# Kernel optimization log

Measured on AMD Instinct MI355X. Metric: run time of the kernel, lower is better.

## Reference

```python
import jax, jax.numpy as jnp
import numpy as np

HIDDEN = 1024
GMM = 16


def setup_inputs() -> dict:
    key = jax.random.key(0)
    ks = jax.random.split(key, 9)
    B, T, D, S = 16, 1024, HIDDEN, 512
    sc_ih = 1.0 / np.sqrt(2 * D)
    sc_hh = 1.0 / np.sqrt(D)
    return {
        "input_h_c": jax.random.normal(ks[0], (B, T, D), jnp.float32),
        "memory": jax.random.normal(ks[1], (B, S, D), jnp.float32),
        "input_lengths": jax.random.randint(ks[2], (B,), 1, S + 1),
        "W_ih": jax.random.uniform(ks[3], (4 * D, 2 * D), jnp.float32, -sc_ih, sc_ih),
        "W_hh": jax.random.uniform(ks[4], (4 * D, D), jnp.float32, -sc_hh, sc_hh),
        "b_ih": jax.random.uniform(ks[5], (4 * D,), jnp.float32, -sc_hh, sc_hh),
        "b_hh": jax.random.uniform(ks[6], (4 * D,), jnp.float32, -sc_hh, sc_hh),
        "Wg_w": jax.random.uniform(ks[7], (3 * GMM, D), jnp.float32, -sc_hh, sc_hh),
        "Wg_b": jax.random.uniform(ks[8], (3 * GMM,), jnp.float32, -sc_hh, sc_hh),
    }


def reference(input_h_c, memory, input_lengths, W_ih, W_hh, b_ih, b_hh, Wg_w, Wg_b):
    B, T, D = input_h_c.shape
    S = memory.shape[1]
    M = Wg_b.shape[0] // 3
    b = b_ih + b_hh
    u = jnp.arange(S, dtype=input_h_c.dtype)  # positions u

    def step(carry, x_t):
        h, c, ctx = carry
        x = jnp.concatenate([x_t, ctx], axis=-1)  # [B, 2D]
        gates = x @ W_ih.T + h @ W_hh.T + b  # [B, 4D], torch gate order i,f,g,o
        i_g, f_g, g_g, o_g = jnp.split(gates, 4, axis=-1)
        c = jax.nn.sigmoid(f_g) * c + jax.nn.sigmoid(i_g) * jnp.tanh(g_g)
        h = jax.nn.sigmoid(o_g) * jnp.tanh(c)
        phi = h @ Wg_w.T + Wg_b  # [B, 3M]
        ksi = jnp.exp(phi[:, :M])
        beta = jnp.exp(phi[:, M:2 * M])
        alpha = jax.nn.softmax(phi[:, 2 * M:], axis=-1)
        # 1/(1+exp((ksi-u)/beta)) == sigmoid((u-ksi)/beta)
        z = (u[None, None, :] - ksi[:, :, None]) / beta[:, :, None]  # [B,M,S]
        half = 0.5 / beta[:, :, None]
        F_R = jax.nn.sigmoid(z + half)  # CDF at u+0.5
        F_L = jax.nn.sigmoid(z - half)  # CDF at u-0.5
        w = jnp.einsum('bm,bms->bs', alpha, F_R - F_L)  # [B,S]
        term = 1.0 - jnp.einsum('bm,bms->bs', alpha, F_R)  # [B,S]
        ctx = jnp.einsum('bs,bsd->bd', w, memory)  # [B,D]
        return (h, c, ctx), (w, term)

    h0 = jnp.zeros((B, D), input_h_c.dtype)
    c0 = jnp.zeros((B, D), input_h_c.dtype)
    ctx0 = jnp.zeros((B, D), input_h_c.dtype)
    (h, c, ctx), (ws, terms) = jax.lax.scan(
        step, (h0, c0, ctx0), jnp.swapaxes(input_h_c, 0, 1))
    alignment = jnp.swapaxes(ws, 0, 1)  # [B,T,S]
    term_last = terms[-1]  # [B,S]
    termination = jnp.take_along_axis(term_last, (input_lengths - 1)[:, None], axis=1)  # [B,1]
    context = ctx[:, None, :]  # [B,1,D], last-step context (as returned by torch forward)
    return (context, alignment, termination)
```

## Files before the change

### kernel.cpp

```cpp
#include <hip/hip_runtime.h>
#include <hip/hip_fp16.h>

#define BB 16
#define TT 1024
#define DD 1024
#define SS 512
#define KK2 2048

#define NBLK 128
#define NTHR 512

#define OUT_ALIGN 16384
#define OUT_TERM  8404992

typedef __attribute__((ext_vector_type(8))) short short8;
typedef __attribute__((ext_vector_type(4))) float floatx4;
typedef __attribute__((ext_vector_type(2))) _Float16 half2v;

struct KParams {
  const float* x;
  const float* mem;
  const int*   lens;
  const float* W_ih;
  const float* W_hh;
  const float* b_ih;
  const float* b_hh;
  const float* Wg_w;
  const float* Wg_b;
  float* out;
  unsigned* bar;
  unsigned short* xc0;
  unsigned short* xc1;
};

__device__ __forceinline__ float sigf(float v) {
  return __builtin_amdgcn_rcpf(1.0f + __expf(-v));
}
__device__ __forceinline__ float tanhfast(float v) {
  float a = fabsf(v);
  float e = __expf(-2.0f * a);
  float r = (1.0f - e) * __builtin_amdgcn_rcpf(1.0f + e);
  return v < 0.0f ? -r : r;
}

__device__ __forceinline__ unsigned short f2bf(float f) {
  unsigned u = __float_as_uint(f);
  return (unsigned short)((u + 0x7FFFu + ((u >> 16) & 1u)) >> 16);
}
__device__ __forceinline__ unsigned pack2bf(float a, float b) {
  return (unsigned)f2bf(a) | ((unsigned)f2bf(b) << 16);
}
__device__ __forceinline__ unsigned cvtpk(float a, float b) {
  unsigned r;
  asm volatile("v_cvt_pk_bf16_f32 %0, %1, %2" : "=v"(r) : "v"(a), "v"(b));
  return r;
}

__device__ __forceinline__ void cstore_u32(unsigned* p2, unsigned v) {
  __hip_atomic_store(p2, v, __ATOMIC_RELAXED, __HIP_MEMORY_SCOPE_AGENT);
}
__device__ __forceinline__ unsigned cload_u32(const unsigned* p2) {
  return __hip_atomic_load(p2, __ATOMIC_RELAXED, __HIP_MEMORY_SCOPE_AGENT);
}
__device__ __forceinline__ unsigned long long cload_u64(const unsigned long long* p2) {
  return __hip_atomic_load(p2, __ATOMIC_RELAXED, __HIP_MEMORY_SCOPE_AGENT);
}

__device__ __forceinline__ void lds_barrier() {
  asm volatile("s_waitcnt lgkmcnt(0)\n\ts_barrier" ::: "memory");
}

__device__ __forceinline__ void grid_barrier(unsigned* bar, unsigned ep, int blk) {
  __syncthreads();
  if (threadIdx.x == 0) cstore_u32(&bar[64 + blk * 32], ep);
  if (threadIdx.x < NBLK) {
    while (cload_u32(&bar[64 + (int)threadIdx.x * 32]) < ep) __builtin_amdgcn_s_sleep(1);
  }
  __syncthreads();
}

union UF { unsigned w[4]; unsigned long long u[2]; short8 s; };

#define MFMA16 __builtin_amdgcn_mfma_f32_16x16x32_bf16

__device__ __forceinline__ void xh_mfma(const UF* xf, const UF* hf, const short8* bfr,
                                        floatx4& a00, floatx4& a01,
                                        floatx4& a10, floatx4& a11) {
  floatx4 z = {0.f, 0.f, 0.f, 0.f};
  a00 = z; a01 = z; a10 = z; a11 = z;
  a00 = MFMA16(xf[0].s, bfr[0],  a00, 0, 0, 0); a01 = MFMA16(xf[1].s, bfr[1],  a01, 0, 0, 0);
  a10 = MFMA16(xf[0].s, bfr[12], a10, 0, 0, 0); a11 = MFMA16(xf[1].s, bfr[13], a11, 0, 0, 0);
  a00 = MFMA16(xf[2].s, bfr[2],  a00, 0, 0, 0); a01 = MFMA16(xf[3].s, bfr[3],  a01, 0, 0, 0);
  a10 = MFMA16(xf[2].s, bfr[14], a10, 0, 0, 0); a11 = MFMA16(xf[3].s, bfr[15], a11, 0, 0, 0);
  a00 = MFMA16(hf[0].s, bfr[8],  a00, 0, 0, 0); a01 = MFMA16(hf[1].s, bfr[9],  a01, 0, 0, 0);
  a10 = MFMA16(hf[0].s, bfr[20], a10, 0, 0, 0); a11 = MFMA16(hf[1].s, bfr[21], a11, 0, 0, 0);
  a00 = MFMA16(hf[2].s, bfr[10], a00, 0, 0, 0); a01 = MFMA16(hf[3].s, bfr[11], a01, 0, 0, 0);
  a10 = MFMA16(hf[2].s, bfr[22], a10, 0, 0, 0); a11 = MFMA16(hf[3].s, bfr[23], a11, 0, 0, 0);
}

__device__ __forceinline__ float sel4(const floatx4& v, int r) {
  return (r == 0) ? v[0] : (r == 1) ? v[1] : (r == 2) ? v[2] : v[3];
}

__global__ __launch_bounds__(NTHR, 2) void tts_kernel(KParams p) {
  extern __shared__ char smem[];
  half2v* memsh2 = (half2v*)smem;

  __shared__ float redC[64 * 65 + 4];
  __shared__ float phiP[384];
  __shared__ float alsh[16], ksish[16], invbsh[16];
  __shared__ float Rsh[513];
  __shared__ half2v wsh2[256];
  __shared__ float ctxp[4][128];
  __shared__ float bsh48[48];

  const int t    = threadIdx.x;
  const int blk  = blockIdx.x;
  const int lane = t & 63;
  const int w    = t >> 6;
  const int bbt  = blk & 15;
  const int dc   = blk >> 4;

  short8 bfr[24];
  {
    const int n = lane & 15;
    const int q = lane >> 4;
#pragma unroll
    for (int nt = 0; nt < 2; ++nt) {
      const int r = (n & 3) * 1024 + blk * 8 + nt * 4 + (n >> 2);
#pragma unroll
      for (int ki = 0; ki < 12; ++ki) {
        short8 v;
        const int k0 = (ki >> 2) * 1024 + w * 128 + (ki & 3) * 32 + q * 8;
#pragma unroll
        for (int j = 0; j < 8; ++j) {
          int k = k0 + j;
          float wv = (k < 2048) ? p.W_ih[(size_t)r * 2048 + k]
                                : p.W_hh[(size_t)r * 1024 + (k - 2048)];
          v[j] = (short)f2bf(wv);
        }
        bfr[nt * 12 + ki] = v;
      }
    }
  }
  short8 wgB[12];
  {
    const int n = lane & 15;
    const int q = lane >> 4;
#pragma unroll
    for (int tau = 0; tau < 3; ++tau)
#pragma unroll
      for (int c = 0; c < 4; ++c) {
        short8 v;
        const float* wg = p.Wg_w + (size_t)(tau * 16 + n) * 1024 + w * 128 + c * 32 + q * 8;
#pragma unroll
        for (int j = 0; j < 8; ++j) v[j] = (short)f2bf(wg[j]);
        wgB[tau * 4 + c] = v;
      }
  }
  float biasreg[4] = {0.f, 0.f, 0.f, 0.f};
  if (t < 128) {
    int dl = t & 7;
#pragma unroll
    for (int g = 0; g < 4; ++g) {
      int r = g * 1024 + blk * 8 + dl;
      biasreg[g] = p.b_ih[r] + p.b_hh[r];
    }
  }
  if (t < 48) bsh48[t] = p.Wg_b[t];
  {
    int dl = t & 127, sp = t >> 7;
    for (int pr = sp; pr < 256; pr += 4) {
      const float* mp = p.mem + (size_t)bbt * SS * DD + (size_t)(2 * pr) * DD + dc * 128 + dl;
      half2v v;
      v.x = (_Float16)mp[0];
      v.y = (_Float16)mp[DD];
      memsh2[pr * 128 + dl] = v;
    }
  }

  float c_val = 0.0f;
  unsigned ep = 0;
  unsigned short* xc_cur = p.xc0;
  unsigned short* xc_nxt = p.xc1;
  const int ab2 = ((lane & 15) * KK2 + w * 128 + ((lane >> 4) * 8)) >> 2;
  const float* xrow = p.x + (size_t)(lane & 15) * TT * DD + w * 128 + ((lane >> 4) * 8);

  floatx4 acc00, acc01, acc10, acc11;
  {
    UF xf[4], hf[4];
#pragma unroll
    for (int sub = 0; sub < 4; ++sub) {
      floatx4 lo = *(const floatx4*)(xrow + sub * 32);
      floatx4 hi = *(const floatx4*)(xrow + sub * 32 + 4);
      xf[sub].w[0] = cvtpk(lo[0], lo[1]); xf[sub].w[1] = cvtpk(lo[2], lo[3]);
      xf[sub].w[2] = cvtpk(hi[0], hi[1]); xf[sub].w[3] = cvtpk(hi[2], hi[3]);
    }
    const unsigned long long* hb = (const unsigned long long*)p.xc0 + ab2 + 256;
#pragma unroll
    for (int sub = 0; sub < 4; ++sub) {
      hf[sub].u[0] = cload_u64(hb + sub * 8);
      hf[sub].u[1] = cload_u64(hb + sub * 8 + 1);
    }
    xh_mfma(xf, hf, bfr, acc00, acc01, acc10, acc11);
  }

  for (int tstep = 0; tstep < TT; ++tstep) {
    {
      const unsigned long long* cb = (const unsigned long long*)xc_cur + ab2;
      UF fc[4];
#pragma unroll
      for (int sub = 0; sub < 4; ++sub) {
        fc[sub].u[0] = cload_u64(cb + sub * 8);
        fc[sub].u[1] = cload_u64(cb + sub * 8 + 1);
      }
      floatx4 c00 = acc00, c01 = acc01, c10 = acc10, c11 = acc11;
      c00 = MFMA16(fc[0].s, bfr[4],  c00, 0, 0, 0); c01 = MFMA16(fc[1].s, bfr[5],  c01, 0, 0, 0);
      c10 = MFMA16(fc[0].s, bfr[16], c10, 0, 0, 0); c11 = MFMA16(fc[1].s, bfr[17], c11, 0, 0, 0);
      c00 = MFMA16(fc[2].s, bfr[6],  c00, 0, 0, 0); c01 = MFMA16(fc[3].s, bfr[7],  c01, 0, 0, 0);
      c10 = MFMA16(fc[2].s, bfr[18], c10, 0, 0, 0); c11 = MFMA16(fc[3].s, bfr[19], c11, 0, 0, 0);
      c00 += c01; c10 += c11;
#pragma unroll
      for (int reg = 0; reg < 4; ++reg) {
        redC[(w * 8 + reg) * 65 + lane]     = c00[reg];
        redC[(w * 8 + 4 + reg) * 65 + lane] = c10[reg];
      }
    }
    lds_barrier();
    if (t < 128) {
      int b = t >> 3, dl = t & 7, nt = dl >> 2, dl4 = dl & 3;
      int row = nt * 4 + (b & 3);
      float gate[4];
#pragma unroll
      for (int g = 0; g < 4; ++g) {
        int ls = ((b >> 2) << 4) | (dl4 * 4 + g);
        float s = biasreg[g];
#pragma unroll
        for (int w2 = 0; w2 < 8; ++w2) s += redC[(w2 * 8 + row) * 65 + ls];
        gate[g] = s;
      }
      c_val = sigf(gate[1]) * c_val + sigf(gate[0]) * tanhfast(gate[2]);
      float hv = sigf(gate[3]) * tanhfast(c_val);
      float hn = __shfl_down(hv, 1, 64);
      if ((t & 1) == 0)
        cstore_u32((unsigned*)(xc_nxt + b * KK2 + 1024 + blk * 8 + dl), pack2bf(hv, hn));
    }
    grid_barrier(p.bar, ++ep, blk);

    UF hf[4];
    {
      const unsigned long long* hb = (const unsigned long long*)xc_nxt + ab2 + 256;
#pragma unroll
      for (int sub = 0; sub < 4; ++sub) {
        hf[sub].u[0] = cload_u64(hb + sub * 8);
        hf[sub].u[1] = cload_u64(hb + sub * 8 + 1);
      }
    }
    UF xf[4];
    if (tstep + 1 < TT) {
      const float* xp = xrow + (size_t)(tstep + 1) * DD;
#pragma unroll
      for (int sub = 0; sub < 4; ++sub) {
        floatx4 lo = *(const floatx4*)(xp + sub * 32);
        floatx4 hi = *(const floatx4*)(xp + sub * 32 + 4);
        xf[sub].w[0] = cvtpk(lo[0], lo[1]); xf[sub].w[1] = cvtpk(lo[2], lo[3]);
        xf[sub].w[2] = cvtpk(hi[0], hi[1]); xf[sub].w[3] = cvtpk(hi[2], hi[3]);
      }
    }
    {
      floatx4 z = {0.f, 0.f, 0.f, 0.f};
      floatx4 ph0 = z, ph1 = z, ph2 = z;
      ph0 = MFMA16(hf[0].s, wgB[0], ph0, 0, 0, 0);
      ph1 = MFMA16(hf[0].s, wgB[4], ph1, 0, 0, 0);
      ph2 = MFMA16(hf[0].s, wgB[8], ph2, 0, 0, 0);
      ph0 = MFMA16(hf[1].s, wgB[1], ph0, 0, 0, 0);
      ph1 = MFMA16(hf[1].s, wgB[5], ph1, 0, 0, 0);
      ph2 = MFMA16(hf[1].s, wgB[9], ph2, 0, 0, 0);
      ph0 = MFMA16(hf[2].s, wgB[2], ph0, 0, 0, 0);
      ph1 = MFMA16(hf[2].s, wgB[6], ph1, 0, 0, 0);
      ph2 = MFMA16(hf[2].s, wgB[10], ph2, 0, 0, 0);
      ph0 = MFMA16(hf[3].s, wgB[3], ph0, 0, 0, 0);
      ph1 = MFMA16(hf[3].s, wgB[7], ph1, 0, 0, 0);
      ph2 = MFMA16(hf[3].s, wgB[11], ph2, 0, 0, 0);
      if ((lane >> 4) == (bbt >> 2)) {
        int m = lane & 15, r = bbt & 3;
        phiP[w * 48 + m]      = sel4(ph0, r);
        phiP[w * 48 + 16 + m] = sel4(ph1, r);
        phiP[w * 48 + 32 + m] = sel4(ph2, r);
      }
    }
    lds_barrier();
    if (t < 64) {
      float s = 0.f;
      if (t < 48) {
        s = bsh48[t];
#pragma unroll
        for (int i = 0; i < 8; ++i) s += phiP[i * 48 + t];
      }
      float mx = s;
#pragma unroll
      for (int o = 1; o < 16; o <<= 1) mx = fmaxf(mx, __shfl_xor(mx, o, 64));
      float e = __expf(s - mx);
      float sm = e;
#pragma unroll
      for (int o = 1; o < 16; o <<= 1) sm += __shfl_xor(sm, o, 64);
      float alpha_v = e * __builtin_amdgcn_rcpf(sm);
      float ksi_v   = __expf(s);
      float invb_v  = __expf(-s);
      if (t >= 32) { if (t < 48) alsh[t - 32] = alpha_v; }
      else if (t < 16) ksish[t] = ksi_v;
      else invbsh[t - 16] = invb_v;
      int m = t & 15;
      float am = __shfl(alpha_v, 32 + m, 64);
      float km = __shfl(ksi_v, m, 64);
      float bm = __shfl(invb_v, 16 + m, 64);
      float term = am * sigf((-0.5f - km) * bm);
#pragma unroll
      for (int o = 1; o < 16; o <<= 1) term += __shfl_xor(term, o, 64);
      if (t == 48) Rsh[0] = term;
    }
    lds_barrier();
    {
      float su = (float)t;
      float rv0 = 0.f, rv1 = 0.f;
#pragma unroll
      for (int m = 0; m < 16; m += 2) {
        rv0 += alsh[m]     * sigf((su + 0.5f - ksish[m])     * invbsh[m]);
        rv1 += alsh[m + 1] * sigf((su + 0.5f - ksish[m + 1]) * invbsh[m + 1]);
      }
      float rv = rv0 + rv1;
      float rvp = __shfl_up(rv, 1, 64);
      float rvn = __shfl_down(rv, 1, 64);
      Rsh[t + 1] = rv;
      if ((t & 1) == 0) {
        half2v v2;
        v2.x = (_Float16)(rv - rvp);
        v2.y = (_Float16)(rvn - rv);
        wsh2[t >> 1] = v2;
      }
      if (dc == 0 && (t & 63) != 0)
        p.out[OUT_ALIGN + ((size_t)bbt * TT + tstep) * SS + t] = rv - rvp;
    }
    lds_barrier();
    {
      if (dc == 0 && t < 8)
        p.out[OUT_ALIGN + ((size_t)bbt * TT + tstep) * SS + 64 * t] =
            Rsh[64 * t + 1] - Rsh[64 * t];
      if (tstep == TT - 1 && dc == 0 && t == 0)
        p.out[OUT_TERM + bbt] = 1.0f - Rsh[p.lens[bbt]];
      int dl = t & 127, sp = t >> 7;
      const int pb = sp * 64;
      half2v wa = wsh2[pb];       wa.x = (_Float16)(Rsh[2 * pb + 1] - Rsh[2 * pb]);
      half2v wb = wsh2[pb + 32];  wb.x = (_Float16)(Rsh[2 * pb + 65] - Rsh[2 * pb + 64]);
      float s0 = __builtin_amdgcn_fdot2(memsh2[pb * 128 + dl], wa, 0.f, false);
      float s1 = __builtin_amdgcn_fdot2(memsh2[(pb + 32) * 128 + dl], wb, 0.f, false);
#pragma unroll 8
      for (int q = 1; q < 32; ++q) {
        s0 = __builtin_amdgcn_fdot2(memsh2[(pb + q) * 128 + dl],      wsh2[pb + q],      s0, false);
        s1 = __builtin_amdgcn_fdot2(memsh2[(pb + 32 + q) * 128 + dl], wsh2[pb + 32 + q], s1, false);
      }
      ctxp[sp][dl] = s0 + s1;
    }
    lds_barrier();
    if (t < 128) {
      float cv = ctxp[0][t] + ctxp[1][t] + ctxp[2][t] + ctxp[3][t];
      if (tstep == TT - 1) p.out[bbt * DD + dc * 128 + t] = cv;
      float cvn = __shfl_down(cv, 1, 64);
      if ((t & 1) == 0)
        cstore_u32((unsigned*)(xc_nxt + bbt * KK2 + dc * 128 + t), pack2bf(cv, cvn));
    }
    __builtin_amdgcn_sched_barrier(0);
    if (tstep + 1 < TT) {
      xh_mfma(xf, hf, bfr, acc00, acc01, acc10, acc11);
    }
    grid_barrier(p.bar, ++ep, blk);

    unsigned short* tmp = xc_cur; xc_cur = xc_nxt; xc_nxt = tmp;
  }
}

extern "C" void kernel_launch(void* const* d_in, const int* in_sizes, int n_in,
                              void* d_out, int out_size, void* d_ws, size_t ws_size,
                              hipStream_t stream) {
  (void)in_sizes; (void)n_in; (void)out_size; (void)ws_size;
  KParams p;
  p.x    = (const float*)d_in[0];
  p.mem  = (const float*)d_in[1];
  p.lens = (const int*)d_in[2];
  p.W_ih = (const float*)d_in[3];
  p.W_hh = (const float*)d_in[4];
  p.b_ih = (const float*)d_in[5];
  p.b_hh = (const float*)d_in[6];
  p.Wg_w = (const float*)d_in[7];
  p.Wg_b = (const float*)d_in[8];
  p.out  = (float*)d_out;
  p.bar  = (unsigned*)d_ws;
  p.xc0  = (unsigned short*)((char*)d_ws + 36864);
  p.xc1  = (unsigned short*)((char*)d_ws + 36864 + 65536);

  hipMemsetAsync(d_ws, 0, 36864 + 65536, stream);

  const unsigned dynLds = 131072;
  hipFuncSetAttribute((const void*)tts_kernel, hipFuncAttributeMaxDynamicSharedMemorySize,
                      (int)dynLds);

  void* args[] = { &p };
  hipLaunchCooperativeKernel((const void*)tts_kernel, dim3(NBLK), dim3(NTHR), args, dynLds,
                             stream);
}
```

Baseline: 13.33 ms.

## Split grid barrier into arrive/wait with master-block release and overlap work

Replaces the all-to-all polling grid barrier with a split arrive/wait scheme. Block 0 polls every block's flag and publishes a single release flag, and the other blocks poll only that flag. The x-load/convert and next-step MFMA work are placed between arrive and wait to hide barrier latency. The gate/LSTM, phi and context-reduction epilogues are compacted into wave 0 so only one wave has to drain its stores before arriving. The cost is an extra hop through block 0 and a serialized single-wave epilogue, and correctness depends on the vmcnt wait being placed right.

```diff
diff --git a/kernel.cpp b/kernel.cpp
--- a/kernel.cpp
+++ b/kernel.cpp
@@ -70,13 +70,29 @@
   asm volatile("s_waitcnt lgkmcnt(0)\n\ts_barrier" ::: "memory");
 }
 
-__device__ __forceinline__ void grid_barrier(unsigned* bar, unsigned ep, int blk) {
-  __syncthreads();
-  if (threadIdx.x == 0) cstore_u32(&bar[64 + blk * 32], ep);
-  if (threadIdx.x < NBLK) {
-    while (cload_u32(&bar[64 + (int)threadIdx.x * 32]) < ep) __builtin_amdgcn_s_sleep(1);
-  }
-  __syncthreads();
+__device__ __forceinline__ void bar_arrive(unsigned* bar, unsigned ep, int blk,
+                                           int w, int lane) {
+  if (w == 0) {
+    asm volatile("s_waitcnt vmcnt(0)" ::: "memory");
+    if (lane == 0) cstore_u32(&bar[64 + blk * 32], ep);
+  }
+}
+__device__ __forceinline__ void bar_wait(unsigned* bar, unsigned ep, int blk,
+                                         int w, int lane) {
+  if (w == 0) {
+    if (blk == 0) {
+      for (;;) {
+        unsigned v0 = cload_u32(&bar[64 + lane * 32]);
+        unsigned v1 = cload_u32(&bar[64 + (lane + 64) * 32]);
+        if (v0 >= ep && v1 >= ep) break;
+        __builtin_amdgcn_s_sleep(1);
+      }
+      if (lane == 0) cstore_u32(&bar[0], ep);
+    } else if (lane == 0) {
+      while (cload_u32(&bar[0]) < ep) __builtin_amdgcn_s_sleep(1);
+    }
+  }
+  lds_barrier();
 }
 
 union UF { unsigned w[4]; unsigned long long u[2]; short8 s; };
@@ -158,14 +174,16 @@
         wgB[tau * 4 + c] = v;
       }
   }
-  float biasreg[4] = {0.f, 0.f, 0.f, 0.f};
-  if (t < 128) {
-    int dl = t & 7;
-#pragma unroll
-    for (int g = 0; g < 4; ++g) {
-      int r = g * 1024 + blk * 8 + dl;
-      biasreg[g] = p.b_ih[r] + p.b_hh[r];
-    }
+  float biasreg[2][4] = {{0.f, 0.f, 0.f, 0.f}, {0.f, 0.f, 0.f, 0.f}};
+  if (w == 0) {
+    int b8 = 2 * (lane & 3);
+#pragma unroll
+    for (int u = 0; u < 2; ++u)
+#pragma unroll
+      for (int g = 0; g < 4; ++g) {
+        int r = g * 1024 + blk * 8 + b8 + u;
+        biasreg[u][g] = p.b_ih[r] + p.b_hh[r];
+      }
   }
   if (t < 48) bsh48[t] = p.Wg_b[t];
   {
@@ -179,7 +197,7 @@
     }
   }
 
-  float c_val = 0.0f;
+  float cval[2] = {0.f, 0.f};
   unsigned ep = 0;
   unsigned short* xc_cur = p.xc0;
   unsigned short* xc_nxt = p.xc1;
@@ -188,21 +206,21 @@
 
   floatx4 acc00, acc01, acc10, acc11;
   {
-    UF xf[4], hf[4];
+    UF xf0[4], hf0[4];
 #pragma unroll
     for (int sub = 0; sub < 4; ++sub) {
       floatx4 lo = *(const floatx4*)(xrow + sub * 32);
       floatx4 hi = *(const floatx4*)(xrow + sub * 32 + 4);
-      xf[sub].w[0] = cvtpk(lo[0], lo[1]); xf[sub].w[1] = cvtpk(lo[2], lo[3]);
-      xf[sub].w[2] = cvtpk(hi[0], hi[1]); xf[sub].w[3] = cvtpk(hi[2], hi[3]);
+      xf0[sub].w[0] = cvtpk(lo[0], lo[1]); xf0[sub].w[1] = cvtpk(lo[2], lo[3]);
+      xf0[sub].w[2] = cvtpk(hi[0], hi[1]); xf0[sub].w[3] = cvtpk(hi[2], hi[3]);
     }
     const unsigned long long* hb = (const unsigned long long*)p.xc0 + ab2 + 256;
 #pragma unroll
     for (int sub = 0; sub < 4; ++sub) {
-      hf[sub].u[0] = cload_u64(hb + sub * 8);
-      hf[sub].u[1] = cload_u64(hb + sub * 8 + 1);
-    }
-    xh_mfma(xf, hf, bfr, acc00, acc01, acc10, acc11);
+      hf0[sub].u[0] = cload_u64(hb + sub * 8);
+      hf0[sub].u[1] = cload_u64(hb + sub * 8 + 1);
+    }
+    xh_mfma(xf0, hf0, bfr, acc00, acc01, acc10, acc11);
   }
 
   for (int tstep = 0; tstep < TT; ++tstep) {
@@ -227,35 +245,29 @@
       }
     }
     lds_barrier();
-    if (t < 128) {
-      int b = t >> 3, dl = t & 7, nt = dl >> 2, dl4 = dl & 3;
-      int row = nt * 4 + (b & 3);
-      float gate[4];
-#pragma unroll
-      for (int g = 0; g < 4; ++g) {
-        int ls = ((b >> 2) << 4) | (dl4 * 4 + g);
-        float s = biasreg[g];
-#pragma unroll
-        for (int w2 = 0; w2 < 8; ++w2) s += redC[(w2 * 8 + row) * 65 + ls];
-        gate[g] = s;
-      }
-      c_val = sigf(gate[1]) * c_val + sigf(gate[0]) * tanhfast(gate[2]);
-      float hv = sigf(gate[3]) * tanhfast(c_val);
-      float hn = __shfl_down(hv, 1, 64);
-      if ((t & 1) == 0)
-        cstore_u32((unsigned*)(xc_nxt + b * KK2 + 1024 + blk * 8 + dl), pack2bf(hv, hn));
-    }
-    grid_barrier(p.bar, ++ep, blk);
-
-    UF hf[4];
-    {
-      const unsigned long long* hb = (const unsigned long long*)xc_nxt + ab2 + 256;
-#pragma unroll
-      for (int sub = 0; sub < 4; ++sub) {
-        hf[sub].u[0] = cload_u64(hb + sub * 8);
-        hf[sub].u[1] = cload_u64(hb + sub * 8 + 1);
-      }
-    }
+    if (w == 0) {
+      int b = lane >> 2, p0 = 2 * (lane & 3);
+      float hv[2];
+#pragma unroll
+      for (int u = 0; u < 2; ++u) {
+        int dl = p0 + u, nt = dl >> 2, dl4 = dl & 3;
+        int row = nt * 4 + (b & 3);
+        float gate[4];
+#pragma unroll
+        for (int g = 0; g < 4; ++g) {
+          int ls = ((b >> 2) << 4) | (dl4 * 4 + g);
+          float s = biasreg[u][g];
+#pragma unroll
+          for (int w2 = 0; w2 < 8; ++w2) s += redC[(w2 * 8 + row) * 65 + ls];
+          gate[g] = s;
+        }
+        cval[u] = sigf(gate[1]) * cval[u] + sigf(gate[0]) * tanhfast(gate[2]);
+        hv[u] = sigf(gate[3]) * tanhfast(cval[u]);
+      }
+      cstore_u32((unsigned*)(xc_nxt + b * KK2 + 1024 + blk * 8 + p0), pack2bf(hv[0], hv[1]));
+    }
+    bar_arrive(p.bar, ++ep, blk, w, lane);
+    __builtin_amdgcn_sched_barrier(0);
     UF xf[4];
     if (tstep + 1 < TT) {
       const float* xp = xrow + (size_t)(tstep + 1) * DD;
@@ -265,6 +277,17 @@
         floatx4 hi = *(const floatx4*)(xp + sub * 32 + 4);
         xf[sub].w[0] = cvtpk(lo[0], lo[1]); xf[sub].w[1] = cvtpk(lo[2], lo[3]);
         xf[sub].w[2] = cvtpk(hi[0], hi[1]); xf[sub].w[3] = cvtpk(hi[2], hi[3]);
+      }
+    }
+    bar_wait(p.bar, ep, blk, w, lane);
+
+    UF hf[4];
+    {
+      const unsigned long long* hb = (const unsigned long long*)xc_nxt + ab2 + 256;
+#pragma unroll
+      for (int sub = 0; sub < 4; ++sub) {
+        hf[sub].u[0] = cload_u64(hb + sub * 8);
+        hf[sub].u[1] = cload_u64(hb + sub * 8 + 1);
       }
     }
     {
@@ -290,12 +313,12 @@
       }
     }
     lds_barrier();
-    if (t < 64) {
+    if (w == 0) {
       float s = 0.f;
-      if (t < 48) {
-        s = bsh48[t];
-#pragma unroll
-        for (int i = 0; i < 8; ++i) s += phiP[i * 48 + t];
+      if (lane < 48) {
+        s = bsh48[lane];
+#pragma unroll
+        for (int i = 0; i < 8; ++i) s += phiP[i * 48 + lane];
       }
       float mx = s;
 #pragma unroll
@@ -307,17 +330,17 @@
       float alpha_v = e * __builtin_amdgcn_rcpf(sm);
       float ksi_v   = __expf(s);
       float invb_v  = __expf(-s);
-      if (t >= 32) { if (t < 48) alsh[t - 32] = alpha_v; }
-      else if (t < 16) ksish[t] = ksi_v;
-      else invbsh[t - 16] = invb_v;
-      int m = t & 15;
+      if (lane >= 32) { if (lane < 48) alsh[lane - 32] = alpha_v; }
+      else if (lane < 16) ksish[lane] = ksi_v;
+      else invbsh[lane - 16] = invb_v;
+      int m = lane & 15;
       float am = __shfl(alpha_v, 32 + m, 64);
       float km = __shfl(ksi_v, m, 64);
       float bm = __shfl(invb_v, 16 + m, 64);
       float term = am * sigf((-0.5f - km) * bm);
 #pragma unroll
       for (int o = 1; o < 16; o <<= 1) term += __shfl_xor(term, o, 64);
-      if (t == 48) Rsh[0] = term;
+      if (lane == 48) Rsh[0] = term;
     }
     lds_barrier();
     {
@@ -362,18 +385,22 @@
       ctxp[sp][dl] = s0 + s1;
     }
     lds_barrier();
-    if (t < 128) {
-      float cv = ctxp[0][t] + ctxp[1][t] + ctxp[2][t] + ctxp[3][t];
-      if (tstep == TT - 1) p.out[bbt * DD + dc * 128 + t] = cv;
-      float cvn = __shfl_down(cv, 1, 64);
-      if ((t & 1) == 0)
-        cstore_u32((unsigned*)(xc_nxt + bbt * KK2 + dc * 128 + t), pack2bf(cv, cvn));
-    }
+    if (w == 0) {
+      int d0 = lane * 2;
+      float cv0 = ctxp[0][d0] + ctxp[1][d0] + ctxp[2][d0] + ctxp[3][d0];
+      float cv1 = ctxp[0][d0 + 1] + ctxp[1][d0 + 1] + ctxp[2][d0 + 1] + ctxp[3][d0 + 1];
+      if (tstep == TT - 1) {
+        p.out[bbt * DD + dc * 128 + d0]     = cv0;
+        p.out[bbt * DD + dc * 128 + d0 + 1] = cv1;
+      }
+      cstore_u32((unsigned*)(xc_nxt + bbt * KK2 + dc * 128 + d0), pack2bf(cv0, cv1));
+    }
+    bar_arrive(p.bar, ++ep, blk, w, lane);
     __builtin_amdgcn_sched_barrier(0);
     if (tstep + 1 < TT) {
       xh_mfma(xf, hf, bfr, acc00, acc01, acc10, acc11);
     }
-    grid_barrier(p.bar, ++ep, blk);
+    bar_wait(p.bar, ep, blk, w, lane);
 
     unsigned short* tmp = xc_cur; xc_cur = xc_nxt; xc_nxt = tmp;
   }
```

Measured after the change: 14.27 ms. 7.0% more time.

## Replace grid barriers with per-element epoch-tagged flag polling on h/ctx

Applied to the files above, without the earlier changes.

Removes the two grid-wide barriers per timestep. Each bf16 pair of h and ctx is now stored as a 64-bit word whose upper half holds the timestep epoch, and consumers poll their own operands until the tag matches, using double-buffered H and C arrays. The next step's x rows are also loaded before the poll so that load latency overlaps the wait. This trades global barrier round trips for data-driven fine-grained waiting, at the cost of doubling the bytes exchanged and adding poll loops on each load.

```diff
diff --git a/kernel.cpp b/kernel.cpp
--- a/kernel.cpp
+++ b/kernel.cpp
@@ -5,7 +5,6 @@
 #define TT 1024
 #define DD 1024
 #define SS 512
-#define KK2 2048
 
 #define NBLK 128
 #define NTHR 512
@@ -28,9 +27,8 @@
   const float* Wg_w;
   const float* Wg_b;
   float* out;
-  unsigned* bar;
-  unsigned short* xc0;
-  unsigned short* xc1;
+  unsigned long long* H;
+  unsigned long long* C;
 };
 
 __device__ __forceinline__ float sigf(float v) {
@@ -56,11 +54,8 @@
   return r;
 }
 
-__device__ __forceinline__ void cstore_u32(unsigned* p2, unsigned v) {
+__device__ __forceinline__ void cstore_u64(unsigned long long* p2, unsigned long long v) {
   __hip_atomic_store(p2, v, __ATOMIC_RELAXED, __HIP_MEMORY_SCOPE_AGENT);
-}
-__device__ __forceinline__ unsigned cload_u32(const unsigned* p2) {
-  return __hip_atomic_load(p2, __ATOMIC_RELAXED, __HIP_MEMORY_SCOPE_AGENT);
 }
 __device__ __forceinline__ unsigned long long cload_u64(const unsigned long long* p2) {
   return __hip_atomic_load(p2, __ATOMIC_RELAXED, __HIP_MEMORY_SCOPE_AGENT);
@@ -70,16 +65,26 @@
   asm volatile("s_waitcnt lgkmcnt(0)\n\ts_barrier" ::: "memory");
 }
 
-__device__ __forceinline__ void grid_barrier(unsigned* bar, unsigned ep, int blk) {
-  __syncthreads();
-  if (threadIdx.x == 0) cstore_u32(&bar[64 + blk * 32], ep);
-  if (threadIdx.x < NBLK) {
-    while (cload_u32(&bar[64 + (int)threadIdx.x * 32]) < ep) __builtin_amdgcn_s_sleep(1);
-  }
-  __syncthreads();
-}
-
 union UF { unsigned w[4]; unsigned long long u[2]; short8 s; };
+
+__device__ __forceinline__ void pollb(const unsigned long long* b, unsigned long long* v,
+                                      unsigned want) {
+#pragma unroll
+  for (int s = 0; s < 4; ++s)
+#pragma unroll
+    for (int j = 0; j < 4; ++j) v[s * 4 + j] = cload_u64(b + s * 16 + j);
+  for (;;) {
+    unsigned bad = 0;
+#pragma unroll
+    for (int i = 0; i < 16; ++i) bad |= ((unsigned)(v[i] >> 32)) ^ want;
+    if (!bad) return;
+    __builtin_amdgcn_s_sleep(2);
+#pragma unroll
+    for (int s = 0; s < 4; ++s)
+#pragma unroll
+      for (int j = 0; j < 4; ++j) v[s * 4 + j] = cload_u64(b + s * 16 + j);
+  }
+}
 
 #define MFMA16 __builtin_amdgcn_mfma_f32_16x16x32_bf16
 
@@ -102,7 +107,7 @@
   return (r == 0) ? v[0] : (r == 1) ? v[1] : (r == 2) ? v[2] : v[3];
 }
 
-__global__ __launch_bounds__(NTHR, 2) void tts_kernel(KParams p) {
+__global__ __launch_bounds__(NTHR, 1) void tts_kernel(KParams p) {
   extern __shared__ char smem[];
   half2v* memsh2 = (half2v*)smem;
 
@@ -179,41 +184,41 @@
     }
   }
 
-  float c_val = 0.0f;
-  unsigned ep = 0;
-  unsigned short* xc_cur = p.xc0;
-  unsigned short* xc_nxt = p.xc1;
-  const int ab2 = ((lane & 15) * KK2 + w * 128 + ((lane >> 4) * 8)) >> 2;
+  float cval = 0.0f;
+  const int eb = (lane & 15) * 512 + w * 64 + (lane >> 4) * 4;
   const float* xrow = p.x + (size_t)(lane & 15) * TT * DD + w * 128 + ((lane >> 4) * 8);
 
   floatx4 acc00, acc01, acc10, acc11;
   {
-    UF xf[4], hf[4];
+    UF xf0[4], hf0[4];
 #pragma unroll
     for (int sub = 0; sub < 4; ++sub) {
       floatx4 lo = *(const floatx4*)(xrow + sub * 32);
       floatx4 hi = *(const floatx4*)(xrow + sub * 32 + 4);
-      xf[sub].w[0] = cvtpk(lo[0], lo[1]); xf[sub].w[1] = cvtpk(lo[2], lo[3]);
-      xf[sub].w[2] = cvtpk(hi[0], hi[1]); xf[sub].w[3] = cvtpk(hi[2], hi[3]);
-    }
-    const unsigned long long* hb = (const unsigned long long*)p.xc0 + ab2 + 256;
-#pragma unroll
-    for (int sub = 0; sub < 4; ++sub) {
-      hf[sub].u[0] = cload_u64(hb + sub * 8);
-      hf[sub].u[1] = cload_u64(hb + sub * 8 + 1);
-    }
-    xh_mfma(xf, hf, bfr, acc00, acc01, acc10, acc11);
+      xf0[sub].w[0] = cvtpk(lo[0], lo[1]); xf0[sub].w[1] = cvtpk(lo[2], lo[3]);
+      xf0[sub].w[2] = cvtpk(hi[0], hi[1]); xf0[sub].w[3] = cvtpk(hi[2], hi[3]);
+    }
+    unsigned long long vh[16];
+    pollb(p.H + 8192 + eb, vh, 0u);
+#pragma unroll
+    for (int sub = 0; sub < 4; ++sub)
+#pragma unroll
+      for (int j = 0; j < 4; ++j) hf0[sub].w[j] = (unsigned)vh[sub * 4 + j];
+    xh_mfma(xf0, hf0, bfr, acc00, acc01, acc10, acc11);
   }
 
   for (int tstep = 0; tstep < TT; ++tstep) {
+    const int q1 = tstep & 1;
+    const int q0 = q1 ^ 1;
+
     {
-      const unsigned long long* cb = (const unsigned long long*)xc_cur + ab2;
+      unsigned long long vc[16];
+      pollb(p.C + q0 * 8192 + eb, vc, (unsigned)tstep);
       UF fc[4];
 #pragma unroll
-      for (int sub = 0; sub < 4; ++sub) {
-        fc[sub].u[0] = cload_u64(cb + sub * 8);
-        fc[sub].u[1] = cload_u64(cb + sub * 8 + 1);
-      }
+      for (int sub = 0; sub < 4; ++sub)
+#pragma unroll
+        for (int j = 0; j < 4; ++j) fc[sub].w[j] = (unsigned)vc[sub * 4 + j];
       floatx4 c00 = acc00, c01 = acc01, c10 = acc10, c11 = acc11;
       c00 = MFMA16(fc[0].s, bfr[4],  c00, 0, 0, 0); c01 = MFMA16(fc[1].s, bfr[5],  c01, 0, 0, 0);
       c10 = MFMA16(fc[0].s, bfr[16], c10, 0, 0, 0); c11 = MFMA16(fc[1].s, bfr[17], c11, 0, 0, 0);
@@ -239,32 +244,41 @@
         for (int w2 = 0; w2 < 8; ++w2) s += redC[(w2 * 8 + row) * 65 + ls];
         gate[g] = s;
       }
-      c_val = sigf(gate[1]) * c_val + sigf(gate[0]) * tanhfast(gate[2]);
-      float hv = sigf(gate[3]) * tanhfast(c_val);
+      cval = sigf(gate[1]) * cval + sigf(gate[0]) * tanhfast(gate[2]);
+      float hv = sigf(gate[3]) * tanhfast(cval);
       float hn = __shfl_down(hv, 1, 64);
       if ((t & 1) == 0)
-        cstore_u32((unsigned*)(xc_nxt + b * KK2 + 1024 + blk * 8 + dl), pack2bf(hv, hn));
-    }
-    grid_barrier(p.bar, ++ep, blk);
-
+        cstore_u64(&p.H[q1 * 8192 + b * 512 + ((blk * 8 + dl) >> 1)],
+                   ((unsigned long long)(tstep + 1) << 32) | pack2bf(hv, hn));
+    }
+
+    floatx4 xlo[4], xhi[4];
+    if (tstep + 1 < TT) {
+      const float* xp = xrow + (size_t)(tstep + 1) * DD;
+#pragma unroll
+      for (int sub = 0; sub < 4; ++sub) {
+        xlo[sub] = *(const floatx4*)(xp + sub * 32);
+        xhi[sub] = *(const floatx4*)(xp + sub * 32 + 4);
+      }
+    }
+    __builtin_amdgcn_sched_barrier(0);
     UF hf[4];
     {
-      const unsigned long long* hb = (const unsigned long long*)xc_nxt + ab2 + 256;
-#pragma unroll
-      for (int sub = 0; sub < 4; ++sub) {
-        hf[sub].u[0] = cload_u64(hb + sub * 8);
-        hf[sub].u[1] = cload_u64(hb + sub * 8 + 1);
-      }
+      unsigned long long vh[16];
+      pollb(p.H + q1 * 8192 + eb, vh, (unsigned)(tstep + 1));
+#pragma unroll
+      for (int sub = 0; sub < 4; ++sub)
+#pragma unroll
+        for (int j = 0; j < 4; ++j) hf[sub].w[j] = (unsigned)vh[sub * 4 + j];
     }
     UF xf[4];
     if (tstep + 1 < TT) {
-      const float* xp = xrow + (size_t)(tstep + 1) * DD;
 #pragma unroll
       for (int sub = 0; sub < 4; ++sub) {
-        floatx4 lo = *(const floatx4*)(xp + sub * 32);
-        floatx4 hi = *(const floatx4*)(xp + sub * 32 + 4);
-        xf[sub].w[0] = cvtpk(lo[0], lo[1]); xf[sub].w[1] = cvtpk(lo[2], lo[3]);
-        xf[sub].w[2] = cvtpk(hi[0], hi[1]); xf[sub].w[3] = cvtpk(hi[2], hi[3]);
+        xf[sub].w[0] = cvtpk(xlo[sub][0], xlo[sub][1]);
+        xf[sub].w[1] = cvtpk(xlo[sub][2], xlo[sub][3]);
+        xf[sub].w[2] = cvtpk(xhi[sub][0], xhi[sub][1]);
+        xf[sub].w[3] = cvtpk(xhi[sub][2], xhi[sub][3]);
       }
     }
     {
@@ -292,10 +306,10 @@
     lds_barrier();
     if (t < 64) {
       float s = 0.f;
-      if (t < 48) {
-        s = bsh48[t];
-#pragma unroll
-        for (int i = 0; i < 8; ++i) s += phiP[i * 48 + t];
+      if (lane < 48) {
+        s = bsh48[lane];
+#pragma unroll
+        for (int i = 0; i < 8; ++i) s += phiP[i * 48 + lane];
       }
       float mx = s;
 #pragma unroll
@@ -307,17 +321,17 @@
       float alpha_v = e * __builtin_amdgcn_rcpf(sm);
       float ksi_v   = __expf(s);
       float invb_v  = __expf(-s);
-      if (t >= 32) { if (t < 48) alsh[t - 32] = alpha_v; }
-      else if (t < 16) ksish[t] = ksi_v;
-      else invbsh[t - 16] = invb_v;
-      int m = t & 15;
+      if (lane >= 32) { if (lane < 48) alsh[lane - 32] = alpha_v; }
+      else if (lane < 16) ksish[lane] = ksi_v;
+      else invbsh[lane - 16] = invb_v;
+      int m = lane & 15;
       float am = __shfl(alpha_v, 32 + m, 64);
       float km = __shfl(ksi_v, m, 64);
       float bm = __shfl(invb_v, 16 + m, 64);
       float term = am * sigf((-0.5f - km) * bm);
 #pragma unroll
       for (int o = 1; o < 16; o <<= 1) term += __shfl_xor(term, o, 64);
-      if (t == 48) Rsh[0] = term;
+      if (lane == 48) Rsh[0] = term;
     }
     lds_barrier();
     {
@@ -367,15 +381,13 @@
       if (tstep == TT - 1) p.out[bbt * DD + dc * 128 + t] = cv;
       float cvn = __shfl_down(cv, 1, 64);
       if ((t & 1) == 0)
-        cstore_u32((unsigned*)(xc_nxt + bbt * KK2 + dc * 128 + t), pack2bf(cv, cvn));
+        cstore_u64(&p.C[q1 * 8192 + bbt * 512 + ((dc * 128 + t) >> 1)],
+                   ((unsigned long long)(tstep + 1) << 32) | pack2bf(cv, cvn));
     }
     __builtin_amdgcn_sched_barrier(0);
     if (tstep + 1 < TT) {
       xh_mfma(xf, hf, bfr, acc00, acc01, acc10, acc11);
     }
-    grid_barrier(p.bar, ++ep, blk);
-
-    unsigned short* tmp = xc_cur; xc_cur = xc_nxt; xc_nxt = tmp;
   }
 }
 
@@ -394,11 +406,10 @@
   p.Wg_w = (const float*)d_in[7];
   p.Wg_b = (const float*)d_in[8];
   p.out  = (float*)d_out;
-  p.bar  = (unsigned*)d_ws;
-  p.xc0  = (unsigned short*)((char*)d_ws + 36864);
-  p.xc1  = (unsigned short*)((char*)d_ws + 36864 + 65536);
-
-  hipMemsetAsync(d_ws, 0, 36864 + 65536, stream);
+  p.H    = (unsigned long long*)d_ws;
+  p.C    = (unsigned long long*)((char*)d_ws + 131072);
+
+  hipMemsetAsync(d_ws, 0, 262144, stream);
 
   const unsigned dynLds = 131072;
   hipFuncSetAttribute((const void*)tts_kernel, hipFuncAttributeMaxDynamicSharedMemorySize,
```

Result: slower. 18.53 ms (+38.9%).
